# Kernel tuning notes

Measured on AMD Instinct MI355X. Metric: run time of the kernel, lower is better.

Reference implementation:

```python
import jax, jax.numpy as jnp
import numpy as np

B, N, M = 32, 65536, 64
IMG = 640.0
POS_THR, NEG_THR = 0.5, 0.4
ALPHA, GAMMA = 0.25, 2.0
BBOX_W = 2.0
EPS = 1e-6


def setup_inputs() -> dict:
    key = jax.random.key(0)
    k1, k2, k3, k4, k5 = jax.random.split(key, 5)
    # predictions: cx, cy in [0, IMG], w, h in [8, 72], obj logit ~ N(0,1)
    cxcy = jax.random.uniform(k1, (B, N, 2), jnp.float32) * IMG
    wh = jax.random.uniform(k2, (B, N, 2), jnp.float32) * 64.0 + 8.0
    obj = jax.random.normal(k3, (B, N, 1), jnp.float32)
    predictions = jnp.concatenate([cxcy, wh, obj], axis=-1)  # [B, N, 5]
    # ground-truth boxes in xyxy, centers in [0, IMG], sizes in [10, 100]
    gcxcy = jax.random.uniform(k4, (B, M, 2), jnp.float32) * IMG
    gwh = jax.random.uniform(k5, (B, M, 2), jnp.float32) * 90.0 + 10.0
    gt_boxes = jnp.concatenate([gcxcy - gwh / 2, gcxcy + gwh / 2], axis=-1)  # [B, M, 4]
    return {"predictions": predictions, "gt_boxes": gt_boxes}


def _focal(logits, targets):
    # stable BCE-with-logits, then focal modulation
    bce = jnp.maximum(logits, 0.0) - logits * targets + jnp.log1p(jnp.exp(-jnp.abs(logits)))
    p = jax.nn.sigmoid(logits)
    p_t = jnp.where(targets == 1.0, p, 1.0 - p)
    alpha_t = jnp.where(targets == 1.0, ALPHA, 1.0 - ALPHA)
    return alpha_t * (1.0 - p_t) ** GAMMA * bce


def _pairwise_iou(pb, gb):
    # pb: [N,4] xyxy, gb: [M,4] xyxy -> [N,M]
    x1 = jnp.maximum(pb[:, None, 0], gb[None, :, 0])
    y1 = jnp.maximum(pb[:, None, 1], gb[None, :, 1])
    x2 = jnp.minimum(pb[:, None, 2], gb[None, :, 2])
    y2 = jnp.minimum(pb[:, None, 3], gb[None, :, 3])
    inter = jnp.clip(x2 - x1, 0.0) * jnp.clip(y2 - y1, 0.0)
    area_p = (pb[:, 2] - pb[:, 0]) * (pb[:, 3] - pb[:, 1])
    area_g = (gb[:, 2] - gb[:, 0]) * (gb[:, 3] - gb[:, 1])
    union = area_p[:, None] + area_g[None, :] - inter
    return inter / jnp.clip(union, EPS)


def _giou_term(pb, gb):
    # elementwise 1 - GIoU; pb, gb: [N,4]
    x1 = jnp.maximum(pb[:, 0], gb[:, 0]); y1 = jnp.maximum(pb[:, 1], gb[:, 1])
    x2 = jnp.minimum(pb[:, 2], gb[:, 2]); y2 = jnp.minimum(pb[:, 3], gb[:, 3])
    inter = jnp.clip(x2 - x1, 0.0) * jnp.clip(y2 - y1, 0.0)
    area_p = (pb[:, 2] - pb[:, 0]) * (pb[:, 3] - pb[:, 1])
    area_g = (gb[:, 2] - gb[:, 0]) * (gb[:, 3] - gb[:, 1])
    union = area_p + area_g - inter
    iou = inter / jnp.clip(union, EPS)
    ex1 = jnp.minimum(pb[:, 0], gb[:, 0]); ey1 = jnp.minimum(pb[:, 1], gb[:, 1])
    ex2 = jnp.maximum(pb[:, 2], gb[:, 2]); ey2 = jnp.maximum(pb[:, 3], gb[:, 3])
    enc = (ex2 - ex1) * (ey2 - ey1)
    giou = iou - (enc - union) / jnp.clip(enc, EPS)
    return 1.0 - giou


def _per_image(pred, gt):
    # pred: [N,5] (cx,cy,w,h,obj), gt: [M,4] xyxy
    cx, cy, w, h = pred[:, 0], pred[:, 1], pred[:, 2], pred[:, 3]
    pb = jnp.stack([cx - w / 2, cy - h / 2, cx + w / 2, cy + h / 2], axis=1)  # decode to xyxy
    obj = pred[:, 4]
    ious = _pairwise_iou(pb, gt)  # [N, M]
    best_pred_per_gt = ious.max(axis=0)              # [M]
    best_pred_idx = jnp.argmax(ious, axis=0)         # [M]
    best_gt_per_pred = ious.max(axis=1)              # [N]
    best_gt_idx = jnp.argmax(ious, axis=1)           # [N]
    # force-match each GT's best anchor if its IoU > 0.1 (scatter-max)
    pos_scatter = jnp.zeros((pred.shape[0],), jnp.int32).at[best_pred_idx].max(
        (best_pred_per_gt > 0.1).astype(jnp.int32))
    pos = (pos_scatter > 0) | (best_gt_per_pred > POS_THR)
    neg = best_gt_per_pred < NEG_THR
    valid = pos | neg
    t = pos.astype(jnp.float32)
    fl = _focal(obj, t)
    vcnt = valid.sum().astype(jnp.float32)
    cls_loss = jnp.where(vcnt > 0, (fl * valid).sum() / jnp.maximum(vcnt, 1.0), 0.0)
    matched = gt[best_gt_idx]                        # [N,4]
    gterm = _giou_term(pb, matched)                  # [N]
    pcnt = pos.sum().astype(jnp.float32)
    reg_loss = jnp.where(pcnt > 0, (gterm * pos).sum() / jnp.maximum(pcnt, 1.0), 0.0)
    return cls_loss, reg_loss, pos.sum()


def reference(predictions, gt_boxes):
    cls_b, reg_b, npos_b = jax.vmap(_per_image)(predictions, gt_boxes)
    num_pos = jnp.maximum(npos_b.sum(), 1).astype(jnp.float32)
    bsz = jnp.float32(predictions.shape[0])
    total_cls = cls_b.sum() / bsz
    total_reg = reg_b.sum() / num_pos * bsz
    return total_cls + BBOX_W * total_reg
```

## Files before the change

### kernel.cpp

```cpp
#include <hip/hip_runtime.h>

#define NB 32
#define NPRED 65536
#define NGT 64
#define BLK 256
#define SLICES 64
#define PPT 4
#define NCB 128
#define CBIN_SCALE 0.2f

#define POS_THR 0.5f
#define NEG_THR 0.4f
#define SCAT_THR 0.1f
#define EPSF 1e-6f


__device__ __forceinline__ int cbin(float x) {
    int bi = (int)(x * CBIN_SCALE);
    return max(0, min(NCB - 1, bi));
}

__device__ __forceinline__ float focal_shared(float l, bool pos) {
    float e  = expf(-fabsf(l));
    float lg = log1pf(e);
    float rp = 1.f / (1.f + e);
    float p  = (l >= 0.f) ? rp : (1.f - rp);
    if (pos) { float q = 1.f - p; return 0.25f * q * q * ((fmaxf(l, 0.f) - l) + lg); }
    return 0.75f * p * p * (fmaxf(l, 0.f) + lg);
}

__device__ __forceinline__ float giou_term(float px1, float py1, float px2, float py2,
                                           float gx1, float gy1, float gx2, float gy2) {
    float x1 = fmaxf(px1, gx1), y1 = fmaxf(py1, gy1);
    float x2 = fminf(px2, gx2), y2 = fminf(py2, gy2);
    float dx = fmaxf(__fsub_rn(x2, x1), 0.f);
    float dy = fmaxf(__fsub_rn(y2, y1), 0.f);
    float inter = __fmul_rn(dx, dy);
    float ap = __fmul_rn(__fsub_rn(px2, px1), __fsub_rn(py2, py1));
    float ag = __fmul_rn(__fsub_rn(gx2, gx1), __fsub_rn(gy2, gy1));
    float uni = __fsub_rn(__fadd_rn(ap, ag), inter);
    float iou = __fdiv_rn(inter, fmaxf(uni, EPSF));
    float ex1 = fminf(px1, gx1), ey1 = fminf(py1, gy1);
    float ex2 = fmaxf(px2, gx2), ey2 = fmaxf(py2, gy2);
    float enc = __fmul_rn(__fsub_rn(ex2, ex1), __fsub_rn(ey2, ey1));
    float giou = __fsub_rn(iou, __fdiv_rn(__fsub_rn(enc, uni), fmaxf(enc, EPSF)));
    return __fsub_rn(1.f, giou);
}


__global__ __launch_bounds__(BLK) void passA(
    const float* __restrict__ pred, const float* __restrict__ gt,
    unsigned long long* __restrict__ keys,
    double* __restrict__ S_fl, double* __restrict__ S_gt,
    int* __restrict__ vcnt, int* __restrict__ pcnt)
{
    const int b = blockIdx.y;
    const int slice = blockIdx.x;
    const int tid = threadIdx.x;
    const int lane = tid & 63;
    const int wv = tid >> 6;

    __shared__ float sgx1[NGT + 1], sgy1[NGT + 1], sgx2[NGT + 1], sgy2[NGT + 1], sgar[NGT + 1];
    __shared__ unsigned long long skey[NGT];
    __shared__ unsigned long long cums[4][NCB];
    __shared__ float rfl[BLK / 64], rgt[BLK / 64];
    __shared__ int rvp[BLK / 64];

    const unsigned base_n = (unsigned)(slice * (BLK * PPT));
    const float4* src4 = (const float4*)(pred + (size_t)b * NPRED * 5 + (size_t)base_n * 5)
                         + (size_t)tid * 5;
    float4 q0 = src4[0], q1 = src4[1], q2 = src4[2], q3 = src4[3], q4 = src4[4];

    const float4* gtb = (const float4*)(gt + (size_t)b * NGT * 4);
    float4 gmine;
    if (tid < NGT) gmine = gtb[tid];
    ((unsigned long long*)cums)[tid] = 0ULL;
    ((unsigned long long*)cums)[tid + BLK] = 0ULL;
    if (tid < NGT) {
        sgx1[tid] = gmine.x; sgy1[tid] = gmine.y;
        sgx2[tid] = gmine.z; sgy2[tid] = gmine.w;
        sgar[tid] = __fmul_rn(__fsub_rn(gmine.z, gmine.x), __fsub_rn(gmine.w, gmine.y));
        skey[tid] = 0ULL;
    } else if (tid == NGT) {
        sgx1[NGT] = 0.f; sgy1[NGT] = 0.f; sgx2[NGT] = 0.f; sgy2[NGT] = 0.f; sgar[NGT] = 0.f;
    }
    __syncthreads();

    if (tid < NGT) {
        unsigned long long bit = 1ULL << tid;
        atomicOr(&cums[0][cbin(gmine.x)], bit);
        atomicOr(&cums[1][cbin(gmine.z)], bit);
        atomicOr(&cums[2][cbin(gmine.y)], bit);
        atomicOr(&cums[3][cbin(gmine.w)], bit);
    }
    __syncthreads();

    {
        unsigned long long v0 = cums[wv][2 * lane];
        unsigned long long v1 = cums[wv][2 * lane + 1];
        unsigned long long v = v0 | v1;
        if ((wv & 1) == 0) {
            #pragma unroll
            for (int off = 1; off < 64; off <<= 1) {
                unsigned long long t = __shfl_up(v, off);
                if (lane >= off) v |= t;
            }
            unsigned long long prev = __shfl_up(v, 1);
            if (lane == 0) prev = 0ULL;
            cums[wv][2 * lane]     = prev | v0;
            cums[wv][2 * lane + 1] = v;
        } else {
            #pragma unroll
            for (int off = 1; off < 64; off <<= 1) {
                unsigned long long t = __shfl_down(v, off);
                if (lane + off < 64) v |= t;
            }
            unsigned long long nxt = __shfl_down(v, 1);
            if (lane == 63) nxt = 0ULL;
            cums[wv][2 * lane]     = v;
            cums[wv][2 * lane + 1] = v1 | nxt;
        }
    }
    __syncthreads();

    const float cxa[PPT] = {q0.x, q1.y, q2.z, q3.w};
    const float cya[PPT] = {q0.y, q1.z, q2.w, q4.x};
    const float wa [PPT] = {q0.z, q1.w, q3.x, q4.y};
    const float ha [PPT] = {q0.w, q2.x, q3.y, q4.z};
    const float oba[PPT] = {q1.x, q2.y, q3.z, q4.w};

    float acc_fl = 0.f, acc_gt = 0.f;
    int acc_vp = 0;

    #pragma unroll
    for (int i = 0; i < PPT; ++i) {
        const float px1 = __fsub_rn(cxa[i], __fmul_rn(wa[i], 0.5f));
        const float py1 = __fsub_rn(cya[i], __fmul_rn(ha[i], 0.5f));
        const float px2 = __fadd_rn(cxa[i], __fmul_rn(wa[i], 0.5f));
        const float py2 = __fadd_rn(cya[i], __fmul_rn(ha[i], 0.5f));
        const float area_p = __fmul_rn(__fsub_rn(px2, px1), __fsub_rn(py2, py1));

        unsigned long long m = (cums[1][cbin(px1)] & cums[0][cbin(px2)])
                             & (cums[3][cbin(py1)] & cums[2][cbin(py2)]);

        const unsigned n = base_n + (unsigned)(PPT * tid + i);
        const unsigned long long nkey = (unsigned long long)(~n);

        float best_iou = 0.f;
        int best_j = 0;

        int j0 = NGT, j1 = NGT;
        if (m) { j0 = __ffsll(m) - 1; m &= m - 1; }
        if (m) { j1 = __ffsll(m) - 1; m &= m - 1; }
        {
            float ax1 = sgx1[j0], ay1 = sgy1[j0], ax2 = sgx2[j0], ay2 = sgy2[j0], aga = sgar[j0];
            float bx1 = sgx1[j1], by1 = sgy1[j1], bx2 = sgx2[j1], by2 = sgy2[j1], agb = sgar[j1];
            float x1 = fmaxf(px1, ax1), y1 = fmaxf(py1, ay1);
            float x2 = fminf(px2, ax2), y2 = fminf(py2, ay2);
            float dx = fmaxf(__fsub_rn(x2, x1), 0.f);
            float dy = fmaxf(__fsub_rn(y2, y1), 0.f);
            float inter = __fmul_rn(dx, dy);
            float uni = __fsub_rn(__fadd_rn(area_p, aga), inter);
            float iou = __fdiv_rn(inter, fmaxf(uni, EPSF));
            iou = (inter > 0.f) ? iou : 0.f;
            if (iou > best_iou) { best_iou = iou; best_j = j0; }
            if (iou > SCAT_THR)
                atomicMax(&skey[j0], (((unsigned long long)__float_as_uint(iou)) << 32) | nkey);

            float X1 = fmaxf(px1, bx1), Y1 = fmaxf(py1, by1);
            float X2 = fminf(px2, bx2), Y2 = fminf(py2, by2);
            float dX = fmaxf(__fsub_rn(X2, X1), 0.f);
            float dY = fmaxf(__fsub_rn(Y2, Y1), 0.f);
            float interB = __fmul_rn(dX, dY);
            float uniB = __fsub_rn(__fadd_rn(area_p, agb), interB);
            float iouB = __fdiv_rn(interB, fmaxf(uniB, EPSF));
            iouB = (interB > 0.f) ? iouB : 0.f;
            if (iouB > best_iou) { best_iou = iouB; best_j = j1; }
            if (iouB > SCAT_THR)
                atomicMax(&skey[j1], (((unsigned long long)__float_as_uint(iouB)) << 32) | nkey);
        }

        while (m) {
            int ja = __ffsll(m) - 1; m &= m - 1;
            int jb = -1;
            if (m) { jb = __ffsll(m) - 1; m &= m - 1; }
            int jbc = (jb >= 0) ? jb : NGT;
            float ax1 = sgx1[ja], ay1 = sgy1[ja], ax2 = sgx2[ja], ay2 = sgy2[ja], aga = sgar[ja];
            float bx1 = sgx1[jbc], by1 = sgy1[jbc], bx2 = sgx2[jbc], by2 = sgy2[jbc], agb = sgar[jbc];
            {
                float x1 = fmaxf(px1, ax1), y1 = fmaxf(py1, ay1);
                float x2 = fminf(px2, ax2), y2 = fminf(py2, ay2);
                float dx = fmaxf(__fsub_rn(x2, x1), 0.f);
                float dy = fmaxf(__fsub_rn(y2, y1), 0.f);
                float inter = __fmul_rn(dx, dy);
                if (inter > 0.f) {
                    float uni = __fsub_rn(__fadd_rn(area_p, aga), inter);
                    float iou = __fdiv_rn(inter, fmaxf(uni, EPSF));
                    if (iou > best_iou) { best_iou = iou; best_j = ja; }
                    if (iou > SCAT_THR)
                        atomicMax(&skey[ja], (((unsigned long long)__float_as_uint(iou)) << 32) | nkey);
                }
            }
            if (jb >= 0) {
                float x1 = fmaxf(px1, bx1), y1 = fmaxf(py1, by1);
                float x2 = fminf(px2, bx2), y2 = fminf(py2, by2);
                float dx = fmaxf(__fsub_rn(x2, x1), 0.f);
                float dy = fmaxf(__fsub_rn(y2, y1), 0.f);
                float inter = __fmul_rn(dx, dy);
                if (inter > 0.f) {
                    float uni = __fsub_rn(__fadd_rn(area_p, agb), inter);
                    float iou = __fdiv_rn(inter, fmaxf(uni, EPSF));
                    if (iou > best_iou) { best_iou = iou; best_j = jb; }
                    if (iou > SCAT_THR)
                        atomicMax(&skey[jb], (((unsigned long long)__float_as_uint(iou)) << 32) | nkey);
                }
            }
        }

        const bool pos0   = best_iou > POS_THR;
        const bool negf   = best_iou < NEG_THR;
        const bool valid0 = pos0 || negf;
        if (valid0) acc_fl += focal_shared(oba[i], pos0);
        if (pos0) {
            acc_gt += giou_term(px1, py1, px2, py2,
                                sgx1[best_j], sgy1[best_j], sgx2[best_j], sgy2[best_j]);
        }
        acc_vp += (valid0 ? 1 : 0) | (pos0 ? 0x10000 : 0);
    }

    for (int off = 32; off; off >>= 1) {
        acc_fl += __shfl_down(acc_fl, off);
        acc_gt += __shfl_down(acc_gt, off);
        acc_vp += __shfl_down(acc_vp, off);
    }
    if (lane == 0) { rfl[wv] = acc_fl; rgt[wv] = acc_gt; rvp[wv] = acc_vp; }
    __syncthreads();
    if (tid == 0) {
        float sfl = 0.f, sgt2 = 0.f; int svp = 0;
        #pragma unroll
        for (int i = 0; i < BLK / 64; ++i) { sfl += rfl[i]; sgt2 += rgt[i]; svp += rvp[i]; }
        atomicAdd(&S_fl[b], (double)sfl);
        atomicAdd(&S_gt[b], (double)sgt2);
        atomicAdd(&vcnt[b], svp & 0xFFFF);
        atomicAdd(&pcnt[b], svp >> 16);
    }
    if (tid < NGT) {
        unsigned long long k = skey[tid];
        if (k) atomicMax(&keys[b * NGT + tid], k);
    }
}


__global__ __launch_bounds__(64) void passBC(
    const float* __restrict__ pred, const float* __restrict__ gt,
    const unsigned long long* __restrict__ keys,
    const double* __restrict__ S_fl, const double* __restrict__ S_gt,
    const int* __restrict__ vcnt, const int* __restrict__ pcnt,
    float* __restrict__ cls_b, float* __restrict__ reg_b, int* __restrict__ npos_b,
    unsigned* __restrict__ done, float* __restrict__ out)
{
    const int b = blockIdx.x;
    const int lane = threadIdx.x;

    __shared__ float4 sgt[NGT];
    __shared__ unsigned cn_list[NGT];

    const float4* gtb = (const float4*)(gt + (size_t)b * NGT * 4);
    float4 gj = gtb[lane];
    sgt[lane] = gj;

    unsigned long long key = keys[b * NGT + lane];
    float miou = __uint_as_float((unsigned)(key >> 32));
    unsigned n = ~((unsigned)(key & 0xFFFFFFFFULL));
    bool qual = miou > SCAT_THR;

    bool unique = qual;
    for (int j2 = 0; j2 < NGT; ++j2) {
        unsigned bn = __shfl(n, j2);
        int bq = __shfl((int)qual, j2);
        if (bq && j2 < lane && bn == n) unique = false;
    }
    unsigned long long mask = __ballot(unique ? 1 : 0);
    int NC = __popcll(mask);
    int slot = __popcll(mask & ((1ULL << lane) - 1ULL));
    if (unique) cn_list[slot] = n;
    __syncthreads();

    float cx = 0.f, cy = 0.f, w = 0.f, h = 0.f, obj = 0.f;
    if (lane < NC) {
        const float* p = pred + (size_t)b * NPRED * 5 + (size_t)cn_list[lane] * 5;
        cx = p[0]; cy = p[1]; w = p[2]; h = p[3]; obj = p[4];
    }
    float px1 = __fsub_rn(cx, __fmul_rn(w, 0.5f));
    float py1 = __fsub_rn(cy, __fmul_rn(h, 0.5f));
    float px2 = __fadd_rn(cx, __fmul_rn(w, 0.5f));
    float py2 = __fadd_rn(cy, __fmul_rn(h, 0.5f));
    float area_p = __fmul_rn(__fsub_rn(px2, px1), __fsub_rn(py2, py1));

    float bv = 0.f; int bj = 0;
    #pragma unroll 4
    for (int j = 0; j < NGT; ++j) {
        float4 g = sgt[j];
        float x1 = fmaxf(px1, g.x), y1 = fmaxf(py1, g.y);
        float x2 = fminf(px2, g.z), y2 = fminf(py2, g.w);
        float dx = fmaxf(__fsub_rn(x2, x1), 0.f);
        float dy = fmaxf(__fsub_rn(y2, y1), 0.f);
        float inter = __fmul_rn(dx, dy);
        if (inter > 0.f) {
            float ag = __fmul_rn(__fsub_rn(g.z, g.x), __fsub_rn(g.w, g.y));
            float uni = __fsub_rn(__fadd_rn(area_p, ag), inter);
            float iou = __fdiv_rn(inter, fmaxf(uni, EPSF));
            if (iou > bv) { bv = iou; bj = j; }
        }
    }

    double add_fl = 0.0, add_gt = 0.0;
    int add_v = 0, add_p = 0;
    if (lane < NC && !(bv > POS_THR)) {
        bool was_neg = bv < NEG_THR;
        float f1 = focal_shared(obj, true);
        float f0 = focal_shared(obj, false);
        add_fl = (double)f1 - (was_neg ? (double)f0 : 0.0);
        add_v = was_neg ? 0 : 1;
        add_p = 1;
        float4 gb = sgt[bj];
        add_gt = (double)giou_term(px1, py1, px2, py2, gb.x, gb.y, gb.z, gb.w);
    }

    for (int off = 32; off; off >>= 1) {
        add_fl += __shfl_down(add_fl, off);
        add_gt += __shfl_down(add_gt, off);
        add_v  += __shfl_down(add_v, off);
        add_p  += __shfl_down(add_p, off);
    }

    if (lane == 0) {
        double sfl = S_fl[b] + add_fl;
        double sgt2 = S_gt[b] + add_gt;
        int v = vcnt[b] + add_v;
        int pc = pcnt[b] + add_p;
        cls_b[b] = (v > 0) ? (float)(sfl / (double)(v > 1 ? v : 1)) : 0.f;
        reg_b[b] = (pc > 0) ? (float)(sgt2 / (double)(pc > 1 ? pc : 1)) : 0.f;
        npos_b[b] = pc;
    }

    __threadfence();
    unsigned t = 0;
    if (lane == 0) t = atomicAdd(done, 1u);
    t = __shfl(t, 0);
    if (t == NB - 1) {
        __threadfence();
        volatile float* vc = cls_b;
        volatile float* vr = reg_b;
        volatile int*   vn = npos_b;
        float cv = (lane < NB) ? vc[lane] : 0.f;
        float rv = (lane < NB) ? vr[lane] : 0.f;
        int   nv = (lane < NB) ? vn[lane] : 0;
        for (int off = 32; off; off >>= 1) {
            cv += __shfl_down(cv, off);
            rv += __shfl_down(rv, off);
            nv += __shfl_down(nv, off);
        }
        if (lane == 0) {
            float num_pos = fmaxf((float)nv, 1.f);
            out[0] = cv / (float)NB + 2.0f * (rv / num_pos * (float)NB);
        }
    }
}


extern "C" void kernel_launch(void* const* d_in, const int* in_sizes, int n_in,
                              void* d_out, int out_size, void* d_ws, size_t ws_size,
                              hipStream_t stream) {
    const float* pred = (const float*)d_in[0];
    const float* gt   = (const float*)d_in[1];
    float* out = (float*)d_out;

    char* ws = (char*)d_ws;
    unsigned long long* keys = (unsigned long long*)(ws + 0);
    double* S_fl   = (double*)(ws + 16384);
    double* S_gt   = (double*)(ws + 16640);
    int* vcnt      = (int*)(ws + 16896);
    int* pcnt      = (int*)(ws + 17024);
    float* cls_b   = (float*)(ws + 17152);
    float* reg_b   = (float*)(ws + 17280);
    int* npos_b    = (int*)(ws + 17408);
    unsigned* done = (unsigned*)(ws + 17536);

    hipMemsetAsync(d_ws, 0, 17664, stream);

    dim3 gridA(SLICES, NB);
    passA<<<gridA, BLK, 0, stream>>>(pred, gt, keys, S_fl, S_gt, vcnt, pcnt);
    passBC<<<NB, 64, 0, stream>>>(pred, gt, keys, S_fl, S_gt, vcnt, pcnt,
                                  cls_b, reg_b, npos_b, done, out);
}
```

Before: 121.0 us.

## Fuse per-image finalization into main pass via last-block-done counter

Merges the second kernel into the main one. Each block writes its partial sums and per-GT keys to per-slice slots instead of using global atomics. The last block to finish an image, detected with a per-image atomic counter, reduces those partials and performs the force-match correction and final loss. This removes one kernel launch and most of the memset, and replaces double atomics with plain stores. The cost is a serial tail in one wavefront per image and a larger workspace.

```diff
diff --git a/kernel.cpp b/kernel.cpp
--- a/kernel.cpp
+++ b/kernel.cpp
@@ -48,11 +48,12 @@
 }
 
 
-__global__ __launch_bounds__(BLK) void passA(
+__global__ __launch_bounds__(BLK) void fused(
     const float* __restrict__ pred, const float* __restrict__ gt,
-    unsigned long long* __restrict__ keys,
-    double* __restrict__ S_fl, double* __restrict__ S_gt,
-    int* __restrict__ vcnt, int* __restrict__ pcnt)
+    unsigned long long* keys2,
+    float* Sfl2, float* Sgt2, int* Svp2,
+    float* cls_b, float* reg_b, int* npos_b,
+    unsigned* done_img, unsigned* done_final, float* out)
 {
     const int b = blockIdx.y;
     const int slice = blockIdx.x;
@@ -65,6 +66,7 @@
     __shared__ unsigned long long cums[4][NCB];
     __shared__ float rfl[BLK / 64], rgt[BLK / 64];
     __shared__ int rvp[BLK / 64];
+    __shared__ unsigned cn_list[NGT];
 
     const unsigned base_n = (unsigned)(slice * (BLK * PPT));
     const float4* src4 = (const float4*)(pred + (size_t)b * NPRED * 5 + (size_t)base_n * 5)
@@ -235,44 +237,36 @@
     }
     if (lane == 0) { rfl[wv] = acc_fl; rgt[wv] = acc_gt; rvp[wv] = acc_vp; }
     __syncthreads();
+
+    const int bs = b * SLICES + slice;
     if (tid == 0) {
-        float sfl = 0.f, sgt2 = 0.f; int svp = 0;
+        float sfl = 0.f, sgt2v = 0.f; int svp = 0;
         #pragma unroll
-        for (int i = 0; i < BLK / 64; ++i) { sfl += rfl[i]; sgt2 += rgt[i]; svp += rvp[i]; }
-        atomicAdd(&S_fl[b], (double)sfl);
-        atomicAdd(&S_gt[b], (double)sgt2);
-        atomicAdd(&vcnt[b], svp & 0xFFFF);
-        atomicAdd(&pcnt[b], svp >> 16);
-    }
-    if (tid < NGT) {
-        unsigned long long k = skey[tid];
-        if (k) atomicMax(&keys[b * NGT + tid], k);
-    }
-}
-
-
-__global__ __launch_bounds__(64) void passBC(
-    const float* __restrict__ pred, const float* __restrict__ gt,
-    const unsigned long long* __restrict__ keys,
-    const double* __restrict__ S_fl, const double* __restrict__ S_gt,
-    const int* __restrict__ vcnt, const int* __restrict__ pcnt,
-    float* __restrict__ cls_b, float* __restrict__ reg_b, int* __restrict__ npos_b,
-    unsigned* __restrict__ done, float* __restrict__ out)
-{
-    const int b = blockIdx.x;
-    const int lane = threadIdx.x;
-
-    __shared__ float4 sgt[NGT];
-    __shared__ unsigned cn_list[NGT];
-
-    const float4* gtb = (const float4*)(gt + (size_t)b * NGT * 4);
-    float4 gj = gtb[lane];
-    sgt[lane] = gj;
-
-    unsigned long long key = keys[b * NGT + lane];
+        for (int i = 0; i < BLK / 64; ++i) { sfl += rfl[i]; sgt2v += rgt[i]; svp += rvp[i]; }
+        Sfl2[bs] = sfl; Sgt2[bs] = sgt2v; Svp2[bs] = svp;
+    }
+    if (tid < NGT) keys2[(size_t)bs * NGT + tid] = skey[tid];
+
+    __threadfence();
+    __syncthreads();
+    unsigned cnt = 0;
+    if (tid == 0) cnt = atomicAdd(&done_img[b], 1u);
+    if (wv != 0) return;
+    cnt = __shfl(cnt, 0);
+    if (cnt != SLICES - 1) return;
+
+    __threadfence();
+
+    const unsigned long long* kb = keys2 + (size_t)b * SLICES * NGT;
+    unsigned long long key = 0ULL;
+    #pragma unroll 8
+    for (int s = 0; s < SLICES; ++s) {
+        unsigned long long k = kb[(size_t)s * NGT + lane];
+        key = (k > key) ? k : key;
+    }
     float miou = __uint_as_float((unsigned)(key >> 32));
     unsigned n = ~((unsigned)(key & 0xFFFFFFFFULL));
-    bool qual = miou > SCAT_THR;
+    bool qual = (miou > SCAT_THR) && (n < NPRED);
 
     bool unique = qual;
     for (int j2 = 0; j2 < NGT; ++j2) {
@@ -284,7 +278,6 @@
     int NC = __popcll(mask);
     int slot = __popcll(mask & ((1ULL << lane) - 1ULL));
     if (unique) cn_list[slot] = n;
-    __syncthreads();
 
     float cx = 0.f, cy = 0.f, w = 0.f, h = 0.f, obj = 0.f;
     if (lane < NC) {
@@ -300,55 +293,54 @@
     float bv = 0.f; int bj = 0;
     #pragma unroll 4
     for (int j = 0; j < NGT; ++j) {
-        float4 g = sgt[j];
-        float x1 = fmaxf(px1, g.x), y1 = fmaxf(py1, g.y);
-        float x2 = fminf(px2, g.z), y2 = fminf(py2, g.w);
+        float gx1 = sgx1[j], gy1 = sgy1[j], gx2 = sgx2[j], gy2 = sgy2[j];
+        float x1 = fmaxf(px1, gx1), y1 = fmaxf(py1, gy1);
+        float x2 = fminf(px2, gx2), y2 = fminf(py2, gy2);
         float dx = fmaxf(__fsub_rn(x2, x1), 0.f);
         float dy = fmaxf(__fsub_rn(y2, y1), 0.f);
         float inter = __fmul_rn(dx, dy);
         if (inter > 0.f) {
-            float ag = __fmul_rn(__fsub_rn(g.z, g.x), __fsub_rn(g.w, g.y));
-            float uni = __fsub_rn(__fadd_rn(area_p, ag), inter);
+            float uni = __fsub_rn(__fadd_rn(area_p, sgar[j]), inter);
             float iou = __fdiv_rn(inter, fmaxf(uni, EPSF));
             if (iou > bv) { bv = iou; bj = j; }
         }
     }
 
-    double add_fl = 0.0, add_gt = 0.0;
-    int add_v = 0, add_p = 0;
+    double c_fl = 0.0, c_gt = 0.0;
+    int c_v = 0, c_p = 0;
     if (lane < NC && !(bv > POS_THR)) {
         bool was_neg = bv < NEG_THR;
         float f1 = focal_shared(obj, true);
         float f0 = focal_shared(obj, false);
-        add_fl = (double)f1 - (was_neg ? (double)f0 : 0.0);
-        add_v = was_neg ? 0 : 1;
-        add_p = 1;
-        float4 gb = sgt[bj];
-        add_gt = (double)giou_term(px1, py1, px2, py2, gb.x, gb.y, gb.z, gb.w);
-    }
-
+        c_fl = (double)f1 - (was_neg ? (double)f0 : 0.0);
+        c_v = was_neg ? 0 : 1;
+        c_p = 1;
+        c_gt = (double)giou_term(px1, py1, px2, py2, sgx1[bj], sgy1[bj], sgx2[bj], sgy2[bj]);
+    }
+    {
+        float sf = Sfl2[b * SLICES + lane];
+        float sg = Sgt2[b * SLICES + lane];
+        int   sv = Svp2[b * SLICES + lane];
+        c_fl += (double)sf; c_gt += (double)sg;
+        c_v += sv & 0xFFFF; c_p += sv >> 16;
+    }
     for (int off = 32; off; off >>= 1) {
-        add_fl += __shfl_down(add_fl, off);
-        add_gt += __shfl_down(add_gt, off);
-        add_v  += __shfl_down(add_v, off);
-        add_p  += __shfl_down(add_p, off);
-    }
-
+        c_fl += __shfl_down(c_fl, off);
+        c_gt += __shfl_down(c_gt, off);
+        c_v  += __shfl_down(c_v, off);
+        c_p  += __shfl_down(c_p, off);
+    }
     if (lane == 0) {
-        double sfl = S_fl[b] + add_fl;
-        double sgt2 = S_gt[b] + add_gt;
-        int v = vcnt[b] + add_v;
-        int pc = pcnt[b] + add_p;
-        cls_b[b] = (v > 0) ? (float)(sfl / (double)(v > 1 ? v : 1)) : 0.f;
-        reg_b[b] = (pc > 0) ? (float)(sgt2 / (double)(pc > 1 ? pc : 1)) : 0.f;
-        npos_b[b] = pc;
+        cls_b[b] = (c_v > 0) ? (float)(c_fl / (double)(c_v > 1 ? c_v : 1)) : 0.f;
+        reg_b[b] = (c_p > 0) ? (float)(c_gt / (double)(c_p > 1 ? c_p : 1)) : 0.f;
+        npos_b[b] = c_p;
     }
 
     __threadfence();
-    unsigned t = 0;
-    if (lane == 0) t = atomicAdd(done, 1u);
-    t = __shfl(t, 0);
-    if (t == NB - 1) {
+    unsigned t2 = 0;
+    if (lane == 0) t2 = atomicAdd(done_final, 1u);
+    t2 = __shfl(t2, 0);
+    if (t2 == NB - 1) {
         __threadfence();
         volatile float* vc = cls_b;
         volatile float* vr = reg_b;
@@ -377,20 +369,19 @@
     float* out = (float*)d_out;
 
     char* ws = (char*)d_ws;
-    unsigned long long* keys = (unsigned long long*)(ws + 0);
-    double* S_fl   = (double*)(ws + 16384);
-    double* S_gt   = (double*)(ws + 16640);
-    int* vcnt      = (int*)(ws + 16896);
-    int* pcnt      = (int*)(ws + 17024);
-    float* cls_b   = (float*)(ws + 17152);
-    float* reg_b   = (float*)(ws + 17280);
-    int* npos_b    = (int*)(ws + 17408);
-    unsigned* done = (unsigned*)(ws + 17536);
-
-    hipMemsetAsync(d_ws, 0, 17664, stream);
-
-    dim3 gridA(SLICES, NB);
-    passA<<<gridA, BLK, 0, stream>>>(pred, gt, keys, S_fl, S_gt, vcnt, pcnt);
-    passBC<<<NB, 64, 0, stream>>>(pred, gt, keys, S_fl, S_gt, vcnt, pcnt,
-                                  cls_b, reg_b, npos_b, done, out);
-}
+    unsigned* done_img   = (unsigned*)(ws + 0);
+    unsigned* done_final = (unsigned*)(ws + 128);
+    unsigned long long* keys2 = (unsigned long long*)(ws + 256);
+    float* Sfl2  = (float*)(ws + 256 + 1048576);
+    float* Sgt2  = (float*)(ws + 256 + 1048576 + 8192);
+    int*   Svp2  = (int*)(ws + 256 + 1048576 + 16384);
+    float* cls_b = (float*)(ws + 256 + 1048576 + 24576);
+    float* reg_b = (float*)(ws + 256 + 1048576 + 24704);
+    int*  npos_b = (int*)(ws + 256 + 1048576 + 24832);
+
+    hipMemsetAsync(d_ws, 0, 256, stream);
+
+    dim3 grid(SLICES, NB);
+    fused<<<grid, BLK, 0, stream>>>(pred, gt, keys2, Sfl2, Sgt2, Svp2,
+                                    cls_b, reg_b, npos_b, done_img, done_final, out);
+}
```

After: 239.8 us. +98.1%, slower.
